# Kernel optimization log

Measured on AMD Instinct MI355X. Metric: run time of the kernel, lower is better.

Reference implementation:

```python
import jax, jax.numpy as jnp
import numpy as np

H = 16      # num_heads
DK = 128    # head_dim_qk
DV = 128    # head_dim_v
HID = 2048  # hidden_size
KS = 4      # conv kernel size


def _causal_dwconv(x, w, b):
    # x: [B, T, C], w: [C, KS], b: [C] -- depthwise causal conv (torch pads KS-1 then slices [:T])
    xc = jnp.transpose(x, (0, 2, 1))  # [B, C, T]
    out = jax.lax.conv_general_dilated(
        xc, w[:, None, :], window_strides=(1,), padding=[(KS - 1, 0)],
        feature_group_count=xc.shape[1], dimension_numbers=('NCH', 'OIH', 'NCH'))
    out = out + b[None, :, None]
    return jnp.transpose(out, (0, 2, 1))


def setup_inputs() -> dict:
    key = jax.random.key(0)
    ks = jax.random.split(key, 16)
    s = 0.02
    inp = {
        'x':   jax.random.normal(ks[0], (4, 2048, HID), jnp.float32),
        'Wq':  jax.random.normal(ks[1], (HID, H * DK), jnp.float32) * s,
        'Wk':  jax.random.normal(ks[2], (HID, H * DK), jnp.float32) * s,
        'Wv':  jax.random.normal(ks[3], (HID, H * DV), jnp.float32) * s,
        'Wa':  jax.random.normal(ks[4], (HID, H), jnp.float32) * s,
        'ba':  jnp.zeros((H,), jnp.float32),
        'Wb':  jax.random.normal(ks[5], (HID, H), jnp.float32) * s,
        'bb':  jnp.zeros((H,), jnp.float32),
        'Wg':  jax.random.normal(ks[6], (HID, H * DV), jnp.float32) * s,
        'Wo':  jax.random.normal(ks[7], (H * DV, HID), jnp.float32) * s,
        'qcw': jax.random.normal(ks[8], (H * DK, KS), jnp.float32) * 0.3,
        'qcb': jnp.zeros((H * DK,), jnp.float32),
        'kcw': jax.random.normal(ks[9], (H * DK, KS), jnp.float32) * 0.3,
        'kcb': jnp.zeros((H * DK,), jnp.float32),
        'vcw': jax.random.normal(ks[10], (H * DV, KS), jnp.float32) * 0.3,
        'vcb': jnp.zeros((H * DV,), jnp.float32),
        'ln_w': jnp.ones((DV,), jnp.float32),
        'ln_b': jnp.zeros((DV,), jnp.float32),
    }
    return inp


def _forward(x, Wq, Wk, Wv, Wa, ba, Wb, bb, Wg, Wo, qcw, qcb, kcw, kcb, vcw, vcb, ln_w, ln_b):
    B, T, _ = x.shape
    q = jax.nn.silu(_causal_dwconv(x @ Wq, qcw, qcb))
    k = jax.nn.silu(_causal_dwconv(x @ Wk, kcw, kcb))
    v = jax.nn.silu(_causal_dwconv(x @ Wv, vcw, vcb))
    q = q.reshape(B, T, H, DK)
    k = k.reshape(B, T, H, DK) * (DK ** -0.5)
    v = v.reshape(B, T, H, DV)
    alpha = jax.nn.sigmoid(x @ Wa + ba)  # [B, T, H]
    beta = jax.nn.sigmoid(x @ Wb + bb)   # [B, T, H]

    # time-major for scan
    qT = jnp.transpose(q, (1, 0, 2, 3))
    kT = jnp.transpose(k, (1, 0, 2, 3))
    vT = jnp.transpose(v, (1, 0, 2, 3))
    aT = jnp.transpose(alpha, (1, 0, 2))
    bT = jnp.transpose(beta, (1, 0, 2))

    def step(S, inps):
        qt, kt, vt, at, bt = inps
        Sk = jnp.einsum('bhvk,bhk->bhv', S, kt)            # S @ k
        err = Sk - vt
        S = at[..., None, None] * S - bt[..., None, None] * (err[..., None] * kt[:, :, None, :])
        ot = jnp.einsum('bhvk,bhk->bhv', S, qt)            # output uses NEW state
        return S, ot

    S0 = jnp.zeros((B, H, DV, DK), x.dtype)
    _, oT = jax.lax.scan(step, S0, (qT, kT, vT, aT, bT))    # [T, B, H, DV]
    o = jnp.transpose(oT, (1, 0, 2, 3))                      # [B, T, H, DV]

    # LayerNorm over head_dim_v (eps=1e-5)
    mu = jnp.mean(o, axis=-1, keepdims=True)
    var = jnp.mean(jnp.square(o - mu), axis=-1, keepdims=True)
    o = (o - mu) * jax.lax.rsqrt(var + 1e-5) * ln_w + ln_b

    g = jax.nn.sigmoid(x @ Wg).reshape(B, T, H, DV)
    o = (o * g).reshape(B, T, H * DV)
    return o @ Wo


def reference(x, Wq, Wk, Wv, Wa, ba, Wb, bb, Wg, Wo, qcw, qcb, kcw, kcb, vcw, vcb, ln_w, ln_b):
    return _forward(x, Wq, Wk, Wv, Wa, ba, Wb, bb, Wg, Wo, qcw, qcb, kcw, kcb, vcw, vcb, ln_w, ln_b)
```

## Files before the change

kernel.cpp:

```cpp
#include <hip/hip_runtime.h>
#include <stdint.h>

#define H_   16
#define DK_  128
#define DV_  128
#define HID_ 2048
#define KS_  4
#define B_   4
#define T_   2048
#define BT_  (B_*T_)
#define QKVC (3*HID_)
#define C_   32
#define RS_  32
#define NC_  (T_/C_)

typedef unsigned short u16;
typedef short  bf16x8 __attribute__((ext_vector_type(8)));
typedef u16    u16x8  __attribute__((ext_vector_type(8)));
typedef u16    u16x4  __attribute__((ext_vector_type(4)));
typedef float  f32x4  __attribute__((ext_vector_type(4)));

__device__ __forceinline__ float b2f(u16 u){
  union { unsigned int i; float f; } v; v.i = ((unsigned int)u) << 16; return v.f;
}
__device__ __forceinline__ u16 f2b(float f){
  unsigned int x = __float_as_uint(f);
  unsigned int r = (x + 0x7FFFu + ((x >> 16) & 1u)) >> 16;
  return (u16)r;
}
__device__ __forceinline__ float sigm(float x){ return 1.0f / (1.0f + __expf(-x)); }

#define MFMA16(a,b,c) __builtin_amdgcn_mfma_f32_16x16x32_bf16((a),(b),(c),0,0,0)

__global__ __launch_bounds__(256) void cvt_x_k(const f32x4* __restrict__ src,
                                               u16x4* __restrict__ dst, int n4)
{
  int i0 = blockIdx.x * 256 + threadIdx.x;
  int stride = gridDim.x * 256;
  for (int i = i0; i < n4; i += stride) {
    f32x4 v = src[i];
    u16x4 r; r[0] = f2b(v[0]); r[1] = f2b(v[1]); r[2] = f2b(v[2]); r[3] = f2b(v[3]);
    dst[i] = r;
  }
}

__global__ __launch_bounds__(256) void cvt_small_k(
    const float* __restrict__ qcw, const float* __restrict__ kcw, const float* __restrict__ vcw,
    const float* __restrict__ qcb, const float* __restrict__ kcb, const float* __restrict__ vcb,
    const float* __restrict__ ba,  const float* __restrict__ bb,
    const float* __restrict__ lnw, const float* __restrict__ lnb,
    u16* __restrict__ canon)
{
  int i = blockIdx.x * 256 + threadIdx.x;
  if (i >= 31008) return;
  float v;
  if (i < 24576) {
    const float* s = (i < 8192) ? qcw : (i < 16384) ? kcw : vcw;
    v = s[i & 8191];
  } else if (i < 30720) {
    int j = i - 24576;
    const float* s = (j < 2048) ? qcb : (j < 4096) ? kcb : vcb;
    v = s[j & 2047];
  } else if (i < 30752) {
    int j = i - 30720;
    v = (j < 16) ? ba[j] : bb[j - 16];
  } else {
    int j = i - 30752;
    v = (j < 128) ? lnw[j] : lnb[j - 128];
  }
  canon[i] = f2b(v);
}

__global__ __launch_bounds__(256) void transpose_b(const float* __restrict__ s0,
                                                   const float* __restrict__ s1,
                                                   const float* __restrict__ s2,
                                                   u16* __restrict__ dst,
                                                   int R, int C)
{
  int z = blockIdx.z;
  const float* src = (z == 0) ? s0 : (z == 1) ? s1 : s2;
  u16* d = dst + (size_t)z * R * C;
  __shared__ u16 t[32][33];
  int bx = blockIdx.x * 32;
  int by = blockIdx.y * 32;
  int lx = threadIdx.x & 31, ly = threadIdx.x >> 5;
  #pragma unroll
  for (int i = 0; i < 4; ++i) {
    int r = by + ly + i * 8, c = bx + lx;
    if (r < R && c < C) t[ly + i * 8][lx] = f2b(src[(size_t)r * C + c]);
  }
  __syncthreads();
  #pragma unroll
  for (int i = 0; i < 4; ++i) {
    int r = bx + ly + i * 8;
    int c = by + lx;
    if (r < C && c < R) d[(size_t)r * R + c] = t[lx][ly + i * 8];
  }
}

__device__ __forceinline__ void gload_lds16(const void* gp, void* lp){
  __builtin_amdgcn_global_load_lds(
      (const __attribute__((address_space(1))) void*)gp,
      (__attribute__((address_space(3))) void*)lp, 16, 0, 0);
}

#define GBM 256
#define GBN 256
#define GBK 64

__global__ __launch_bounds__(512, 2) void gemm256(const u16* __restrict__ A, int lda,
                                                  const u16* __restrict__ Bt, int ldb,
                                                  void* __restrict__ C, int ldc,
                                                  int K, int out_f32)
{
  __shared__ u16 lsA[2][GBM * GBK];
  __shared__ u16 lsB[2][GBN * GBK];
  int tid = threadIdx.x, wid = tid >> 6, lane = tid & 63;
  int l16 = lane & 15, quad = lane >> 4;
  int wr = wid >> 2, wc = wid & 3;

  int nbx = gridDim.x;
  int nwg = nbx * gridDim.y;
  int flat = blockIdx.y * nbx + blockIdx.x;
  int swzid = ((nwg & 7) == 0) ? ((flat & 7) * (nwg >> 3) + (flat >> 3)) : flat;
  int m0 = (swzid / nbx) * GBM;
  int n0 = (swzid % nbx) * GBN;

  f32x4 acc[8][4] = {};

  auto STAGE = [&](int t, int bi){
    int k0 = t * GBK;
    #pragma unroll
    for (int ld = 0; ld < 4; ++ld) {
      int slot = ld * 512 + tid;
      int row = slot >> 3, cg = slot & 7;
      int lofs = (ld * 512 + wid * 64) * 8;
      gload_lds16(A  + (size_t)(m0 + row) * lda + k0 + cg * 8, &lsA[bi][lofs]);
      gload_lds16(Bt + (size_t)(n0 + row) * ldb + k0 + cg * 8, &lsB[bi][lofs]);
    }
  };

  STAGE(0, 0);
  __syncthreads();

  int NT = K / GBK;
  for (int t = 0; t < NT; ++t) {
    int bi = t & 1;
    if (t + 1 < NT) STAGE(t + 1, bi ^ 1);
    const u16* pA = lsA[bi];
    const u16* pB = lsB[bi];
    #pragma unroll
    for (int ks = 0; ks < 2; ++ks) {
      bf16x8 bfr[4];
      #pragma unroll
      for (int ni = 0; ni < 4; ++ni)
        bfr[ni] = *(const bf16x8*)&pB[(wc * 64 + ni * 16 + l16) * GBK + ks * 32 + quad * 8];
      #pragma unroll
      for (int mi = 0; mi < 8; ++mi) {
        bf16x8 af = *(const bf16x8*)&pA[(wr * 128 + mi * 16 + l16) * GBK + ks * 32 + quad * 8];
        #pragma unroll
        for (int ni = 0; ni < 4; ++ni)
          acc[mi][ni] = MFMA16(af, bfr[ni], acc[mi][ni]);
      }
    }
    __syncthreads();
  }

  #pragma unroll
  for (int mi = 0; mi < 8; ++mi)
    #pragma unroll
    for (int ni = 0; ni < 4; ++ni)
      #pragma unroll
      for (int r = 0; r < 4; ++r) {
        int m = m0 + wr * 128 + mi * 16 + quad * 4 + r;
        int n = n0 + wc * 64 + ni * 16 + l16;
        if (out_f32) ((float*)C)[(size_t)m * ldc + n] = acc[mi][ni][r];
        else         ((u16*)C)[(size_t)m * ldc + n] = f2b(acc[mi][ni][r]);
      }
}

__global__ __launch_bounds__(256) void ab_k(const u16* __restrict__ x,
                                            const u16* __restrict__ WabT,
                                            const u16* __restrict__ ba,
                                            const u16* __restrict__ bb,
                                            float* __restrict__ ab)
{
  int j = threadIdx.x & 31, rl = threadIdx.x >> 5;
  int row = blockIdx.x * 8 + rl;
  const u16x8* xr = (const u16x8*)(x + (size_t)row * HID_);
  const u16x8* wr = (const u16x8*)(WabT + (size_t)j * HID_);
  float acc = 0.f;
  for (int k = 0; k < HID_ / 8; ++k) {
    u16x8 xv = xr[k], wv = wr[k];
    #pragma unroll
    for (int i = 0; i < 8; ++i) acc += b2f(xv[i]) * b2f(wv[i]);
  }
  float bias = (j < 16) ? b2f(ba[j]) : b2f(bb[j - 16]);
  float sg = sigm(acc + bias);
  if (j < 16) ab[(size_t)row * 16 + j] = sg;
  else        ab[(size_t)BT_ * 16 + (size_t)row * 16 + (j - 16)] = sg;
}

__global__ __launch_bounds__(256) void conv_silu_k(const u16* __restrict__ in,
                                                   const u16* __restrict__ cwv,
                                                   const u16* __restrict__ cbv,
                                                   u16* __restrict__ out)
{
  int idx  = blockIdx.x * 256 + threadIdx.x;
  int col8 = idx % (QKVC / 8);
  int t    = idx / (QKVC / 8);
  int col  = col8 * 8;
  int s = col >> 11;

  u16 wl[32];
  #pragma unroll
  for (int i = 0; i < 4; ++i)
    *(u16x8*)(wl + i * 8) = *(const u16x8*)(cwv + (size_t)col * KS_ + i * 8);
  u16x8 bv = *(const u16x8*)(cbv + col);

  float acc[8];
  #pragma unroll
  for (int j = 0; j < 8; ++j) acc[j] = b2f(bv[j]);

  #pragma unroll
  for (int tap = 0; tap < KS_; ++tap) {
    int tt = t - 3 + tap;
    if (tt >= 0) {
      u16x8 xv = *(const u16x8*)(in + (size_t)tt * QKVC + col);
      #pragma unroll
      for (int j = 0; j < 8; ++j) acc[j] = fmaf(b2f(xv[j]), b2f(wl[j * 4 + tap]), acc[j]);
    }
  }
  float scale = (s == 1) ? 0.08838834764831845f : 1.0f;
  u16x8 rv;
  #pragma unroll
  for (int j = 0; j < 8; ++j) {
    float a = acc[j];
    rv[j] = f2b(a * sigm(a) * scale);
  }
  *(u16x8*)(out + (size_t)t * QKVC + col) = rv;
}

__global__ __launch_bounds__(512) void chunk_scan_k(const u16* __restrict__ qkv,
                                                    const float* __restrict__ ab,
                                                    u16* __restrict__ o)
{
  __shared__ __align__(16) char smem[64896];
  u16 (*Kim)[136] = (u16(*)[136])(smem);
  u16 (*Qim)[136] = (u16(*)[136])(smem + 8704);
  u16 (*Sh)[136]  = (u16(*)[136])(smem + 17408);
  u16 (*Sl)[136]  = (u16(*)[136])(smem + 26112);
  u16 (*KT)[40]   = (u16(*)[40])(smem + 34816);
  u16 (*Vim)[32]  = (u16(*)[32])(smem + 45056);
  float (*KK)[36] = (float(*)[36])(smem + 47104);
  float (*KQ)[33] = (float(*)[33])(smem + 51712);
  float (*SK0)[33]= (float(*)[33])(smem + 55936);
  float (*SQ0)[33]= (float(*)[33])(smem + 60160);
  float (*PL4)[4] = (float(*)[4])(smem + 64384);
  float (*U)[33]  = (float(*)[33])(smem + 8704);

  int bid = blockIdx.x;
  int chain = bid & 63, rblk = bid >> 6;
  int b = chain >> 4, h = chain & 15;
  int tid = threadIdx.x, wv = tid >> 6, lane = tid & 63;
  int l16 = lane & 15, quad = lane >> 4;

  const u16* kbase = qkv + (size_t)b * T_ * QKVC + HID_ + h * DK_;
  const u16* qbase = qkv + (size_t)b * T_ * QKVC + h * DK_;
  const u16* vbase = qkv + (size_t)b * T_ * QKVC + 2 * HID_ + h * DV_ + rblk * RS_;
  const float* abase = ab + (size_t)b * T_ * 16 + h;
  const float* bbase = abase + (size_t)BT_ * 16;
  u16* obase = o + (size_t)b * T_ * 2048 + h * DV_ + rblk * RS_;

  f32x4 st[2];
  #pragma unroll
  for (int rt = 0; rt < 2; ++rt)
    #pragma unroll
    for (int r = 0; r < 4; ++r) st[rt][r] = 0.f;

  int jb = tid - 64;
  u16x8 stg[3];
  float avp = 0.f;

  auto LD = [&](int c) {
    int t0 = c * C_;
    if (wv == 0) {
      avp = (lane < 32) ? abase[(size_t)(t0 + lane) * 16]
                        : bbase[(size_t)(t0 + lane - 32) * 16];
    } else {
      #pragma unroll
      for (int it = 0; it < 3; ++it) {
        int j = jb + it * 448;
        if (j < 512) {
          int t = j >> 4, g = j & 15;
          stg[it] = *(const u16x8*)(kbase + (size_t)(t0 + t) * QKVC + g * 8);
        } else if (j < 1024) {
          int j2 = j - 512, t = j2 >> 4, g = j2 & 15;
          stg[it] = *(const u16x8*)(qbase + (size_t)(t0 + t) * QKVC + g * 8);
        } else if (j < 1152) {
          int j2 = j - 1024, t = j2 >> 2, rg = j2 & 3;
          stg[it] = *(const u16x8*)(vbase + (size_t)(t0 + t) * QKVC + rg * 8);
        }
      }
    }
  };

  LD(0);

  for (int c = 0; c < NC_; ++c) {
    int t0 = c * C_;

    #pragma unroll
    for (int rt = 0; rt < 2; ++rt)
      #pragma unroll
      for (int r = 0; r < 4; ++r) {
        float s = st[rt][r];
        u16 hi = f2b(s);
        float lo = s - b2f(hi);
        int row = rt * 16 + quad * 4 + r;
        int col = wv * 16 + l16;
        Sh[row][col] = hi;
        Sl[row][col] = f2b(lo);
      }

    if (wv == 0) {
      float av = avp;
      float p = av;
      #pragma unroll
      for (int d = 1; d < 32; d <<= 1) {
        float up = __shfl_up(p, d);
        if (lane >= d && lane < 32) p *= up;
      }
      float pm1 = __shfl_up(p, 1);
      float bt = __shfl(av, lane + 32);
      if (lane < 32) {
        if (lane == 0) pm1 = 1.f;
        f32x4 g;
        g[0] = bt * pm1; g[1] = bt; g[2] = 1.0f / p; g[3] = p;
        *(f32x4*)PL4[lane] = g;
      }
    } else {
      #pragma unroll
      for (int it = 0; it < 3; ++it) {
        int j = jb + it * 448;
        if (j < 512) {
          int t = j >> 4, g = j & 15;
          *(u16x8*)&Kim[t][g * 8] = stg[it];
          int blk = ((t >> 3) ^ (g & 3)) << 3;
          int tl = t & 7;
          #pragma unroll
          for (int e = 0; e < 8; ++e)
            KT[g * 8 + e][blk + tl] = stg[it][e];
        } else if (j < 1024) {
          int j2 = j - 512, t = j2 >> 4, g = j2 & 15;
          *(u16x8*)&Qim[t][g * 8] = stg[it];
        } else if (j < 1152) {
          int j2 = j - 1024, t = j2 >> 2, rg = j2 & 3;
          *(u16x8*)&Vim[t][rg * 8] = stg[it];
        }
      }
    }
    if (c + 1 < NC_) LD(c + 1);
    __syncthreads();

    {
      auto dotKK = [&](int mt, int nt) {
        f32x4 acc = {0.f,0.f,0.f,0.f};
        #pragma unroll
        for (int ks = 0; ks < 4; ++ks) {
          bf16x8 A = *(const bf16x8*)&Kim[mt * 16 + l16][ks * 32 + quad * 8];
          bf16x8 B = *(const bf16x8*)&Kim[nt * 16 + l16][ks * 32 + quad * 8];
          acc = MFMA16(A, B, acc);
        }
        #pragma unroll
        for (int r = 0; r < 4; ++r) KK[mt * 16 + quad * 4 + r][nt * 16 + l16] = acc[r];
      };
      auto dotKQ = [&](int mt, int nt) {
        f32x4 acc = {0.f,0.f,0.f,0.f};
        #pragma unroll
        for (int ks = 0; ks < 4; ++ks) {
          bf16x8 A = *(const bf16x8*)&Qim[mt * 16 + l16][ks * 32 + quad * 8];
          bf16x8 B = *(const bf16x8*)&Kim[nt * 16 + l16][ks * 32 + quad * 8];
          acc = MFMA16(A, B, acc);
        }
        #pragma unroll
        for (int r = 0; r < 4; ++r) KQ[mt * 16 + quad * 4 + r][nt * 16 + l16] = acc[r];
      };
      auto dotS = [&](const u16 (*Aarr)[136], int tt, int rr, float (*OUT)[33]) {
        f32x4 acc = {0.f,0.f,0.f,0.f};
        #pragma unroll
        for (int ks = 0; ks < 4; ++ks) {
          bf16x8 A  = *(const bf16x8*)&Aarr[tt * 16 + l16][ks * 32 + quad * 8];
          bf16x8 Bh = *(const bf16x8*)&Sh[rr * 16 + l16][ks * 32 + quad * 8];
          bf16x8 Bl = *(const bf16x8*)&Sl[rr * 16 + l16][ks * 32 + quad * 8];
          acc = MFMA16(A, Bh, acc);
          acc = MFMA16(A, Bl, acc);
        }
        #pragma unroll
        for (int r = 0; r < 4; ++r) OUT[tt * 16 + quad * 4 + r][rr * 16 + l16] = acc[r];
      };
      switch (wv) {
        case 0: dotS(Kim, 0, 0, SK0); dotKK(0, 0); break;
        case 1: dotS(Kim, 0, 1, SK0); dotKK(1, 0); break;
        case 2: dotS(Kim, 1, 0, SK0); dotKK(1, 1); break;
        case 3: dotS(Kim, 1, 1, SK0); dotKQ(0, 0); break;
        case 4: dotS(Qim, 0, 0, SQ0); dotKQ(1, 0); break;
        case 5: dotS(Qim, 0, 1, SQ0); dotKQ(1, 1); break;
        case 6: dotS(Qim, 1, 0, SQ0); break;
        default: dotS(Qim, 1, 1, SQ0); break;
      }
    }
    __syncthreads();

    union { u16x8 u; bf16x8 b; } gh, gl;
    int omt = (wv - 4) >> 1, ont = (wv - 4) & 1;
    if (wv == 0) {
      if (lane < 32) {
        float ub[C_];
        #pragma unroll
        for (int t = 0; t < C_; ++t) {
          f32x4 g = *(const f32x4*)PL4[t];
          float u = g[0] * SK0[t][lane] - g[1] * b2f(Vim[t][lane]);
          float acc = 0.f;
          #pragma unroll
          for (int i4 = 0; i4 < t / 4; ++i4) {
            f32x4 kk = *(const f32x4*)&KK[t][i4 * 4];
            acc = fmaf(kk[0], ub[i4 * 4 + 0], acc);
            acc = fmaf(kk[1], ub[i4 * 4 + 1], acc);
            acc = fmaf(kk[2], ub[i4 * 4 + 2], acc);
            acc = fmaf(kk[3], ub[i4 * 4 + 3], acc);
          }
          #pragma unroll
          for (int i = (t / 4) * 4; i < t; ++i)
            acc = fmaf(KK[t][i], ub[i], acc);
          u = fmaf(-g[0], acc, u);
          U[t][lane] = u;
          ub[t] = g[2] * u;
        }
      }
    } else if (wv >= 4) {
      int trow = omt * 16 + l16;
      float Pt = PL4[trow][3];
      #pragma unroll
      for (int e = 0; e < 8; ++e) {
        int i = quad * 8 + e;
        float gv = (i <= trow) ? (-Pt * PL4[i][2] * KQ[trow][i]) : 0.f;
        u16 h2 = f2b(gv);
        gh.u[e] = h2; gl.u[e] = f2b(gv - b2f(h2));
      }
    }
    __syncthreads();

    {
      float PL31 = PL4[31][3];

      #pragma unroll
      for (int rt = 0; rt < 2; ++rt) {
        union { u16x8 u; bf16x8 b; } ah, al;
        #pragma unroll
        for (int e = 0; e < 8; ++e) {
          int i = quad * 8 + e;
          float uv = U[i][rt * 16 + l16];
          float ucv = -PL31 * PL4[i][2] * uv;
          u16 hh = f2b(ucv);
          ah.u[e] = hh; al.u[e] = f2b(ucv - b2f(hh));
        }
        int col = wv * 16 + l16;
        bf16x8 Bk = *(const bf16x8*)&KT[col][(quad ^ ((col >> 3) & 3)) << 3];
        f32x4 cacc;
        #pragma unroll
        for (int r = 0; r < 4; ++r) cacc[r] = PL31 * st[rt][r];
        cacc = MFMA16(ah.b, Bk, cacc);
        cacc = MFMA16(al.b, Bk, cacc);
        st[rt] = cacc;
      }

      if (wv >= 4) {
        union { u16x8 u; bf16x8 b; } uth, utl;
        #pragma unroll
        for (int e = 0; e < 8; ++e) {
          int i = quad * 8 + e;
          float uv = U[i][ont * 16 + l16];
          u16 h1 = f2b(uv);
          uth.u[e] = h1; utl.u[e] = f2b(uv - b2f(h1));
        }
        f32x4 oacc;
        #pragma unroll
        for (int r = 0; r < 4; ++r) {
          int t = omt * 16 + quad * 4 + r;
          oacc[r] = PL4[t][3] * SQ0[t][ont * 16 + l16];
        }
        oacc = MFMA16(gh.b, uth.b, oacc);
        oacc = MFMA16(gh.b, utl.b, oacc);
        oacc = MFMA16(gl.b, uth.b, oacc);
        #pragma unroll
        for (int r = 0; r < 4; ++r) {
          int t = omt * 16 + quad * 4 + r;
          obase[(size_t)(t0 + t) * 2048 + ont * 16 + l16] = f2b(oacc[r]);
        }
      }
    }
    __syncthreads();
  }
}

__global__ __launch_bounds__(256) void ln_gate_k(const u16* __restrict__ o_raw,
                                                 const u16* __restrict__ g,
                                                 const u16* __restrict__ lnw,
                                                 const u16* __restrict__ lnb,
                                                 u16* __restrict__ o_ln)
{
  int gid = blockIdx.x * 4 + (threadIdx.x >> 6);
  int lane = threadIdx.x & 63;
  int row = gid >> 4, h = gid & 15;
  size_t ofs = (size_t)row * 2048 + h * 128 + lane * 2;
  unsigned int e2 = *(const unsigned int*)(o_raw + ofs);
  float ex = b2f((u16)(e2 & 0xffff)), ey = b2f((u16)(e2 >> 16));
  float s = ex + ey, ss = ex * ex + ey * ey;
  #pragma unroll
  for (int m = 1; m < 64; m <<= 1) { s += __shfl_xor(s, m); ss += __shfl_xor(ss, m); }
  float mean = s * (1.f / 128.f);
  float var  = ss * (1.f / 128.f) - mean * mean;
  float rstd = rsqrtf(fmaxf(var, 0.f) + 1e-5f);
  float w0 = b2f(lnw[lane * 2]), w1 = b2f(lnw[lane * 2 + 1]);
  float b0 = b2f(lnb[lane * 2]), b1 = b2f(lnb[lane * 2 + 1]);
  unsigned int g2 = *(const unsigned int*)(g + ofs);
  float g0 = sigm(b2f((u16)(g2 & 0xffff))), g1 = sigm(b2f((u16)(g2 >> 16)));
  float r0 = ((ex - mean) * rstd * w0 + b0) * g0;
  float r1 = ((ey - mean) * rstd * w1 + b1) * g1;
  *(unsigned int*)(o_ln + ofs) = (unsigned int)f2b(r0) | ((unsigned int)f2b(r1) << 16);
}

extern "C" void kernel_launch(void* const* d_in, const int* in_sizes, int n_in,
                              void* d_out, int out_size, void* d_ws, size_t ws_size,
                              hipStream_t stream)
{
  const float* x   = (const float*)d_in[0];
  const float* Wq  = (const float*)d_in[1];
  const float* Wk  = (const float*)d_in[2];
  const float* Wv  = (const float*)d_in[3];
  const float* Wa  = (const float*)d_in[4];
  const float* ba  = (const float*)d_in[5];
  const float* Wb  = (const float*)d_in[6];
  const float* bb  = (const float*)d_in[7];
  const float* Wg  = (const float*)d_in[8];
  const float* Wo  = (const float*)d_in[9];
  const float* qcw = (const float*)d_in[10];
  const float* qcb = (const float*)d_in[11];
  const float* kcw = (const float*)d_in[12];
  const float* kcb = (const float*)d_in[13];
  const float* vcw = (const float*)d_in[14];
  const float* vcb = (const float*)d_in[15];
  const float* lnw = (const float*)d_in[16];
  const float* lnb = (const float*)d_in[17];
  (void)in_sizes; (void)n_in; (void)out_size;

  char* ws = (char*)d_ws;
  size_t off = 0;
  auto alloc = [&](size_t bytes) -> void* {
    void* p = ws + off; off += (bytes + 255) & ~(size_t)255; return p;
  };
  u16* WT    = (u16*)alloc((size_t)3 * HID_ * HID_ * 2);
  u16* WabT  = (u16*)alloc((size_t)32 * HID_ * 2);
  u16* xc    = (u16*)alloc((size_t)BT_ * HID_ * 2);
  u16* canon = (u16*)alloc((size_t)31008 * 2);
  u16* post  = (u16*)alloc((size_t)BT_ * QKVC * 2);
  float* abuf = (float*)alloc((size_t)2 * BT_ * 16 * 4);
  size_t base_off = off;

  size_t fused_need = base_off + (((size_t)BT_ * QKVC * 2 + 255) & ~(size_t)255);
  int fused = (fused_need <= ws_size);
  u16* preC;
  if (fused) preC = (u16*)alloc((size_t)BT_ * QKVC * 2);
  else       preC = (u16*)alloc((size_t)BT_ * HID_ * 2 * 2);
  if (off > ws_size) return;

  u16* cw_c  = canon;
  u16* cb_c  = canon + 24576;
  u16* ba_c  = canon + 30720;
  u16* bb_c  = canon + 30736;
  u16* lnw_c = canon + 30752;
  u16* lnb_c = canon + 30880;

  u16* o_raw = preC;
  u16* g_raw = post;
  u16* o_ln  = post + (size_t)BT_ * HID_;
  u16* WTg   = WT;

  dim3 tb(256), tb5(512);

  cvt_x_k<<<dim3(4096), tb, 0, stream>>>((const f32x4*)x, (u16x4*)xc, BT_ * HID_ / 4);
  cvt_small_k<<<dim3(122), tb, 0, stream>>>(qcw, kcw, vcw, qcb, kcb, vcb, ba, bb, lnw, lnb, canon);

  transpose_b<<<dim3(64, 64, 3), tb, 0, stream>>>(Wq, Wk, Wv, WT, HID_, HID_);
  transpose_b<<<dim3(1, 64, 2), tb, 0, stream>>>(Wa, Wb, Wb, WabT, HID_, 16);

  if (fused) {
    gemm256<<<dim3(QKVC / GBN, BT_ / GBM), tb5, 0, stream>>>(xc, HID_, WT, HID_, preC, QKVC, HID_, 0);
    for (int b = 0; b < B_; ++b)
      conv_silu_k<<<dim3(T_ * (QKVC / 8) / 256), tb, 0, stream>>>(
          preC + (size_t)b * T_ * QKVC, cw_c, cb_c, post + (size_t)b * T_ * QKVC);
  } else {
    for (int b = 0; b < B_; ++b) {
      const u16* xb = xc + (size_t)b * T_ * HID_;
      gemm256<<<dim3(QKVC / GBN, T_ / GBM), tb5, 0, stream>>>(xb, HID_, WT, HID_, preC, QKVC, HID_, 0);
      conv_silu_k<<<dim3(T_ * (QKVC / 8) / 256), tb, 0, stream>>>(
          preC, cw_c, cb_c, post + (size_t)b * T_ * QKVC);
    }
  }

  transpose_b<<<dim3(64, 64, 2), tb, 0, stream>>>(Wg, Wo, Wo, WTg, HID_, HID_);

  ab_k<<<dim3(BT_ / 8), tb, 0, stream>>>(xc, WabT, ba_c, bb_c, abuf);

  chunk_scan_k<<<dim3(256), tb5, 0, stream>>>(post, abuf, o_raw);

  gemm256<<<dim3(HID_ / GBN, BT_ / GBM), tb5, 0, stream>>>(xc, HID_, WTg, HID_, g_raw, HID_, HID_, 0);

  ln_gate_k<<<dim3(BT_ * H_ / 4), tb, 0, stream>>>(o_raw, g_raw, lnw_c, lnb_c, o_ln);

  gemm256<<<dim3(HID_ / GBN, BT_ / GBM), tb5, 0, stream>>>(o_ln, HID_,
      WT + (size_t)HID_ * HID_, HID_, d_out, HID_, HID_, 1);
}
```

Before: 1.233 ms.

## Split chunk-scan state rows into 16-row slices, two chains per block

Cuts the per-block V-row slice from 32 to 16. Each 512-thread block now runs two independent chains in separate 4-wave groups, each with its own shared-memory region, and the intra-chunk work is redistributed across the four waves of a group. The aim is to double the number of concurrent chain slices, which shortens the serial per-lane triangular solve and raises parallelism on the sequential scan. In exchange, the K/Q loads and the KK/KQ products are duplicated across twice as many row slices, shared memory grows to about 100KB per block, and the next-chunk prefetch now waits until after the barrier.

```diff
diff --git a/kernel.cpp b/kernel.cpp
--- a/kernel.cpp
+++ b/kernel.cpp
@@ -11,7 +11,7 @@
 #define BT_  (B_*T_)
 #define QKVC (3*HID_)
 #define C_   32
-#define RS_  32
+#define RS_  16
 #define NC_  (T_/C_)
 
 typedef unsigned short u16;
@@ -245,25 +245,29 @@
                                                     const float* __restrict__ ab,
                                                     u16* __restrict__ o)
 {
-  __shared__ __align__(16) char smem[64896];
-  u16 (*Kim)[136] = (u16(*)[136])(smem);
-  u16 (*Qim)[136] = (u16(*)[136])(smem + 8704);
-  u16 (*Sh)[136]  = (u16(*)[136])(smem + 17408);
-  u16 (*Sl)[136]  = (u16(*)[136])(smem + 26112);
-  u16 (*KT)[40]   = (u16(*)[40])(smem + 34816);
-  u16 (*Vim)[32]  = (u16(*)[32])(smem + 45056);
-  float (*KK)[36] = (float(*)[36])(smem + 47104);
-  float (*KQ)[33] = (float(*)[33])(smem + 51712);
-  float (*SK0)[33]= (float(*)[33])(smem + 55936);
-  float (*SQ0)[33]= (float(*)[33])(smem + 60160);
-  float (*PL4)[4] = (float(*)[4])(smem + 64384);
-  float (*U)[33]  = (float(*)[33])(smem + 8704);
-
+  __shared__ __align__(16) char smem[102144];
   int bid = blockIdx.x;
-  int chain = bid & 63, rblk = bid >> 6;
+  int tid = threadIdx.x, wv = tid >> 6, lane = tid & 63;
+  int grp = wv >> 2, wl = wv & 3;
+  int l16 = lane & 15, quad = lane >> 4;
+
+  char* gs = smem + grp * 51072;
+  u16 (*Kim)[136] = (u16(*)[136])(gs);
+  u16 (*Qim)[136] = (u16(*)[136])(gs + 8704);
+  u16 (*Sh)[136]  = (u16(*)[136])(gs + 17408);
+  u16 (*Sl)[136]  = (u16(*)[136])(gs + 21760);
+  u16 (*KT)[40]   = (u16(*)[40])(gs + 26112);
+  u16 (*Vim)[16]  = (u16(*)[16])(gs + 36352);
+  float (*KK)[36] = (float(*)[36])(gs + 37376);
+  float (*KQ)[33] = (float(*)[33])(gs + 41984);
+  float (*SK0)[17]= (float(*)[17])(gs + 46208);
+  float (*SQ0)[17]= (float(*)[17])(gs + 48384);
+  float (*PL4)[4] = (float(*)[4])(gs + 50560);
+  float (*U)[17]  = (float(*)[17])(gs + 8704);
+
+  int chain = grp * 32 + (bid & 31);
+  int rblk = bid >> 5;
   int b = chain >> 4, h = chain & 15;
-  int tid = threadIdx.x, wv = tid >> 6, lane = tid & 63;
-  int l16 = lane & 15, quad = lane >> 4;
 
   const u16* kbase = qkv + (size_t)b * T_ * QKVC + HID_ + h * DK_;
   const u16* qbase = qkv + (size_t)b * T_ * QKVC + h * DK_;
@@ -274,31 +278,31 @@
 
   f32x4 st[2];
   #pragma unroll
-  for (int rt = 0; rt < 2; ++rt)
+  for (int ct = 0; ct < 2; ++ct)
     #pragma unroll
-    for (int r = 0; r < 4; ++r) st[rt][r] = 0.f;
-
-  int jb = tid - 64;
-  u16x8 stg[3];
+    for (int r = 0; r < 4; ++r) st[ct][r] = 0.f;
+
+  int jb = (wl - 1) * 64 + lane;
+  u16x8 stg[6];
   float avp = 0.f;
 
   auto LD = [&](int c) {
     int t0 = c * C_;
-    if (wv == 0) {
+    if (wl == 0) {
       avp = (lane < 32) ? abase[(size_t)(t0 + lane) * 16]
                         : bbase[(size_t)(t0 + lane - 32) * 16];
     } else {
       #pragma unroll
-      for (int it = 0; it < 3; ++it) {
-        int j = jb + it * 448;
+      for (int it = 0; it < 6; ++it) {
+        int j = jb + it * 192;
         if (j < 512) {
           int t = j >> 4, g = j & 15;
           stg[it] = *(const u16x8*)(kbase + (size_t)(t0 + t) * QKVC + g * 8);
         } else if (j < 1024) {
           int j2 = j - 512, t = j2 >> 4, g = j2 & 15;
           stg[it] = *(const u16x8*)(qbase + (size_t)(t0 + t) * QKVC + g * 8);
-        } else if (j < 1152) {
-          int j2 = j - 1024, t = j2 >> 2, rg = j2 & 3;
+        } else if (j < 1088) {
+          int j2 = j - 1024, t = j2 >> 1, rg = j2 & 1;
           stg[it] = *(const u16x8*)(vbase + (size_t)(t0 + t) * QKVC + rg * 8);
         }
       }
@@ -311,19 +315,19 @@
     int t0 = c * C_;
 
     #pragma unroll
-    for (int rt = 0; rt < 2; ++rt)
+    for (int ct = 0; ct < 2; ++ct)
       #pragma unroll
       for (int r = 0; r < 4; ++r) {
-        float s = st[rt][r];
+        float s = st[ct][r];
         u16 hi = f2b(s);
         float lo = s - b2f(hi);
-        int row = rt * 16 + quad * 4 + r;
-        int col = wv * 16 + l16;
+        int row = quad * 4 + r;
+        int col = wl * 32 + ct * 16 + l16;
         Sh[row][col] = hi;
         Sl[row][col] = f2b(lo);
       }
 
-    if (wv == 0) {
+    if (wl == 0) {
       float av = avp;
       float p = av;
       #pragma unroll
@@ -341,8 +345,8 @@
       }
     } else {
       #pragma unroll
-      for (int it = 0; it < 3; ++it) {
-        int j = jb + it * 448;
+      for (int it = 0; it < 6; ++it) {
+        int j = jb + it * 192;
         if (j < 512) {
           int t = j >> 4, g = j & 15;
           *(u16x8*)&Kim[t][g * 8] = stg[it];
@@ -354,14 +358,14 @@
         } else if (j < 1024) {
           int j2 = j - 512, t = j2 >> 4, g = j2 & 15;
           *(u16x8*)&Qim[t][g * 8] = stg[it];
-        } else if (j < 1152) {
-          int j2 = j - 1024, t = j2 >> 2, rg = j2 & 3;
+        } else if (j < 1088) {
+          int j2 = j - 1024, t = j2 >> 1, rg = j2 & 1;
           *(u16x8*)&Vim[t][rg * 8] = stg[it];
         }
       }
     }
+    __syncthreads();
     if (c + 1 < NC_) LD(c + 1);
-    __syncthreads();
 
     {
       auto dotKK = [&](int mt, int nt) {
@@ -386,36 +390,32 @@
         #pragma unroll
         for (int r = 0; r < 4; ++r) KQ[mt * 16 + quad * 4 + r][nt * 16 + l16] = acc[r];
       };
-      auto dotS = [&](const u16 (*Aarr)[136], int tt, int rr, float (*OUT)[33]) {
+      auto dotS = [&](const u16 (*Aarr)[136], int tt, float (*OUT)[17]) {
         f32x4 acc = {0.f,0.f,0.f,0.f};
         #pragma unroll
         for (int ks = 0; ks < 4; ++ks) {
           bf16x8 A  = *(const bf16x8*)&Aarr[tt * 16 + l16][ks * 32 + quad * 8];
-          bf16x8 Bh = *(const bf16x8*)&Sh[rr * 16 + l16][ks * 32 + quad * 8];
-          bf16x8 Bl = *(const bf16x8*)&Sl[rr * 16 + l16][ks * 32 + quad * 8];
+          bf16x8 Bh = *(const bf16x8*)&Sh[l16][ks * 32 + quad * 8];
+          bf16x8 Bl = *(const bf16x8*)&Sl[l16][ks * 32 + quad * 8];
           acc = MFMA16(A, Bh, acc);
           acc = MFMA16(A, Bl, acc);
         }
         #pragma unroll
-        for (int r = 0; r < 4; ++r) OUT[tt * 16 + quad * 4 + r][rr * 16 + l16] = acc[r];
+        for (int r = 0; r < 4; ++r) OUT[tt * 16 + quad * 4 + r][l16] = acc[r];
       };
-      switch (wv) {
-        case 0: dotS(Kim, 0, 0, SK0); dotKK(0, 0); break;
-        case 1: dotS(Kim, 0, 1, SK0); dotKK(1, 0); break;
-        case 2: dotS(Kim, 1, 0, SK0); dotKK(1, 1); break;
-        case 3: dotS(Kim, 1, 1, SK0); dotKQ(0, 0); break;
-        case 4: dotS(Qim, 0, 0, SQ0); dotKQ(1, 0); break;
-        case 5: dotS(Qim, 0, 1, SQ0); dotKQ(1, 1); break;
-        case 6: dotS(Qim, 1, 0, SQ0); break;
-        default: dotS(Qim, 1, 1, SQ0); break;
+      switch (wl) {
+        case 0: dotS(Kim, 0, SK0); dotKK(0, 0); dotKK(1, 0); break;
+        case 1: dotS(Kim, 1, SK0); dotKK(1, 1); dotKQ(0, 0); break;
+        case 2: dotS(Qim, 0, SQ0); dotKQ(1, 0); dotKQ(1, 1); break;
+        default: dotS(Qim, 1, SQ0); break;
       }
     }
     __syncthreads();
 
     union { u16x8 u; bf16x8 b; } gh, gl;
-    int omt = (wv - 4) >> 1, ont = (wv - 4) & 1;
-    if (wv == 0) {
-      if (lane < 32) {
+    int omt = wl - 2;
+    if (wl == 0) {
+      if (lane < 16) {
         float ub[C_];
         #pragma unroll
         for (int t = 0; t < C_; ++t) {
@@ -438,7 +438,7 @@
           ub[t] = g[2] * u;
         }
       }
-    } else if (wv >= 4) {
+    } else if (wl >= 2) {
       int trow = omt * 16 + l16;
       float Pt = PL4[trow][3];
       #pragma unroll
@@ -454,33 +454,33 @@
     {
       float PL31 = PL4[31][3];
 
-      #pragma unroll
-      for (int rt = 0; rt < 2; ++rt) {
-        union { u16x8 u; bf16x8 b; } ah, al;
+      union { u16x8 u; bf16x8 b; } ah, al;
+      #pragma unroll
+      for (int e = 0; e < 8; ++e) {
+        int i = quad * 8 + e;
+        float uv = U[i][l16];
+        float ucv = -PL31 * PL4[i][2] * uv;
+        u16 hh = f2b(ucv);
+        ah.u[e] = hh; al.u[e] = f2b(ucv - b2f(hh));
+      }
+      #pragma unroll
+      for (int ct = 0; ct < 2; ++ct) {
+        int col = wl * 32 + ct * 16 + l16;
+        bf16x8 Bk = *(const bf16x8*)&KT[col][(quad ^ ((col >> 3) & 3)) << 3];
+        f32x4 cacc;
+        #pragma unroll
+        for (int r = 0; r < 4; ++r) cacc[r] = PL31 * st[ct][r];
+        cacc = MFMA16(ah.b, Bk, cacc);
+        cacc = MFMA16(al.b, Bk, cacc);
+        st[ct] = cacc;
+      }
+
+      if (wl >= 2) {
+        union { u16x8 u; bf16x8 b; } uth, utl;
         #pragma unroll
         for (int e = 0; e < 8; ++e) {
           int i = quad * 8 + e;
-          float uv = U[i][rt * 16 + l16];
-          float ucv = -PL31 * PL4[i][2] * uv;
-          u16 hh = f2b(ucv);
-          ah.u[e] = hh; al.u[e] = f2b(ucv - b2f(hh));
-        }
-        int col = wv * 16 + l16;
-        bf16x8 Bk = *(const bf16x8*)&KT[col][(quad ^ ((col >> 3) & 3)) << 3];
-        f32x4 cacc;
-        #pragma unroll
-        for (int r = 0; r < 4; ++r) cacc[r] = PL31 * st[rt][r];
-        cacc = MFMA16(ah.b, Bk, cacc);
-        cacc = MFMA16(al.b, Bk, cacc);
-        st[rt] = cacc;
-      }
-
-      if (wv >= 4) {
-        union { u16x8 u; bf16x8 b; } uth, utl;
-        #pragma unroll
-        for (int e = 0; e < 8; ++e) {
-          int i = quad * 8 + e;
-          float uv = U[i][ont * 16 + l16];
+          float uv = U[i][l16];
           u16 h1 = f2b(uv);
           uth.u[e] = h1; utl.u[e] = f2b(uv - b2f(h1));
         }
@@ -488,7 +488,7 @@
         #pragma unroll
         for (int r = 0; r < 4; ++r) {
           int t = omt * 16 + quad * 4 + r;
-          oacc[r] = PL4[t][3] * SQ0[t][ont * 16 + l16];
+          oacc[r] = PL4[t][3] * SQ0[t][l16];
         }
         oacc = MFMA16(gh.b, uth.b, oacc);
         oacc = MFMA16(gh.b, utl.b, oacc);
@@ -496,7 +496,7 @@
         #pragma unroll
         for (int r = 0; r < 4; ++r) {
           int t = omt * 16 + quad * 4 + r;
-          obase[(size_t)(t0 + t) * 2048 + ont * 16 + l16] = f2b(oacc[r]);
+          obase[(size_t)(t0 + t) * 2048 + l16] = f2b(oacc[r]);
         }
       }
     }
```

Measured after the change: 1.366 ms. +10.7%, slower.

## Triple-buffer GEMM LDS staging with XOR swizzle and vmcnt-based barriers

Applied to the files above, without the earlier changes.

The bf16 GEMM now uses a K tile of 32 with three LDS buffers, prefetching two tiles ahead. Waits use explicit s_waitcnt vmcnt counts plus s_barrier instead of __syncthreads, so the next tile's loads can stay in flight while the current one computes. Global-to-LDS placement and LDS reads use an XOR swizzle on 16-byte chunks to cut bank conflicts. The costs are twice as many loop iterations and barriers, and the hand-counted vmcnt values must exactly match the number of outstanding loads.

```diff
diff --git a/kernel.cpp b/kernel.cpp
--- a/kernel.cpp
+++ b/kernel.cpp
@@ -106,15 +106,15 @@
 
 #define GBM 256
 #define GBN 256
-#define GBK 64
+#define GBK 32
 
 __global__ __launch_bounds__(512, 2) void gemm256(const u16* __restrict__ A, int lda,
                                                   const u16* __restrict__ Bt, int ldb,
                                                   void* __restrict__ C, int ldc,
                                                   int K, int out_f32)
 {
-  __shared__ u16 lsA[2][GBM * GBK];
-  __shared__ u16 lsB[2][GBN * GBK];
+  __shared__ u16 lsA[3][GBM * GBK];
+  __shared__ u16 lsB[3][GBN * GBK];
   int tid = threadIdx.x, wid = tid >> 6, lane = tid & 63;
   int l16 = lane & 15, quad = lane >> 4;
   int wr = wid >> 2, wc = wid & 3;
@@ -131,39 +131,48 @@
   auto STAGE = [&](int t, int bi){
     int k0 = t * GBK;
     #pragma unroll
-    for (int ld = 0; ld < 4; ++ld) {
+    for (int ld = 0; ld < 2; ++ld) {
       int slot = ld * 512 + tid;
-      int row = slot >> 3, cg = slot & 7;
+      int row = slot >> 2, ch = slot & 3;
+      int gcol = (ch ^ ((row >> 1) & 3)) * 8;
       int lofs = (ld * 512 + wid * 64) * 8;
-      gload_lds16(A  + (size_t)(m0 + row) * lda + k0 + cg * 8, &lsA[bi][lofs]);
-      gload_lds16(Bt + (size_t)(n0 + row) * ldb + k0 + cg * 8, &lsB[bi][lofs]);
+      gload_lds16(A  + (size_t)(m0 + row) * lda + k0 + gcol, &lsA[bi][lofs]);
+      gload_lds16(Bt + (size_t)(n0 + row) * ldb + k0 + gcol, &lsB[bi][lofs]);
     }
   };
 
+  int NT = K / GBK;
   STAGE(0, 0);
-  __syncthreads();
-
-  int NT = K / GBK;
+  STAGE(1, 1);
+  asm volatile("s_waitcnt vmcnt(4)" ::: "memory");
+  __builtin_amdgcn_s_barrier();
+
   for (int t = 0; t < NT; ++t) {
-    int bi = t & 1;
-    if (t + 1 < NT) STAGE(t + 1, bi ^ 1);
+    int bi = t % 3;
+    if (t + 2 < NT) STAGE(t + 2, (bi + 2) % 3);
     const u16* pA = lsA[bi];
     const u16* pB = lsB[bi];
-    #pragma unroll
-    for (int ks = 0; ks < 2; ++ks) {
+    {
       bf16x8 bfr[4];
       #pragma unroll
-      for (int ni = 0; ni < 4; ++ni)
-        bfr[ni] = *(const bf16x8*)&pB[(wc * 64 + ni * 16 + l16) * GBK + ks * 32 + quad * 8];
+      for (int ni = 0; ni < 4; ++ni) {
+        int row = wc * 64 + ni * 16 + l16;
+        bfr[ni] = *(const bf16x8*)&pB[row * GBK + ((quad ^ ((row >> 1) & 3)) * 8)];
+      }
       #pragma unroll
       for (int mi = 0; mi < 8; ++mi) {
-        bf16x8 af = *(const bf16x8*)&pA[(wr * 128 + mi * 16 + l16) * GBK + ks * 32 + quad * 8];
+        int row = wr * 128 + mi * 16 + l16;
+        bf16x8 af = *(const bf16x8*)&pA[row * GBK + ((quad ^ ((row >> 1) & 3)) * 8)];
         #pragma unroll
         for (int ni = 0; ni < 4; ++ni)
           acc[mi][ni] = MFMA16(af, bfr[ni], acc[mi][ni]);
       }
     }
-    __syncthreads();
+    if (t + 1 < NT) {
+      if (t + 2 < NT) asm volatile("s_waitcnt vmcnt(4)" ::: "memory");
+      else            asm volatile("s_waitcnt vmcnt(0)" ::: "memory");
+      __builtin_amdgcn_s_barrier();
+    }
   }
 
   #pragma unroll
```

Result: no change. 1.258 ms (+2.0%).
